# Kernel tuning notes

Hardware: AMD Instinct MI355X
Metric: run time of the kernel (lower is better)

The kernel has to match this reference:

```python
import jax, jax.numpy as jnp
import numpy as np

B, L = 2, 1024
V, D_MODEL, NL = 32, 256, 6
DI, DS, DC, DTR = 512, 16, 4, 16  # d_inner=expand*d_model, d_state, d_conv, dt_rank=d_model/16
NC, MAXL = 10, 2048
ALPHA = 0.1  # observer_alpha


def setup_inputs() -> dict:
    key = jax.random.key(0)
    ks = jax.random.split(key, 16)
    std = 0.02
    emb = std * jax.random.normal(ks[0], (V, D_MODEL), jnp.float32)
    emb = emb.at[0].set(0.0)  # padding_idx=0
    pos_emb = std * jax.random.normal(ks[1], (MAXL, D_MODEL), jnp.float32)
    ln_w = jnp.ones((NL, D_MODEL), jnp.float32)
    ln_b = jnp.zeros((NL, D_MODEL), jnp.float32)
    in_proj_w = std * jax.random.normal(ks[2], (NL, 2 * DI, D_MODEL), jnp.float32)
    conv_w = 0.1 * jax.random.normal(ks[3], (NL, DI, DC), jnp.float32)
    conv_b = jnp.zeros((NL, DI), jnp.float32)
    x_proj_w = std * jax.random.normal(ks[4], (NL, DTR + 2 * DS, DI), jnp.float32)
    dt_proj_w = std * jax.random.normal(ks[5], (NL, DI, DTR), jnp.float32)
    dt_proj_b = jnp.full((NL, DI), -4.6, jnp.float32)  # softplus(-4.6) ~ 0.01 init dt
    A_log = jnp.broadcast_to(jnp.log(jnp.arange(1, DS + 1, dtype=jnp.float32)), (NL, DI, DS)).copy()  # S4D-real
    Dp = jnp.ones((NL, DI), jnp.float32)
    out_proj_w = std * jax.random.normal(ks[6], (NL, D_MODEL, DI), jnp.float32)
    norm_w = jnp.ones((D_MODEL,), jnp.float32)
    norm_b = jnp.zeros((D_MODEL,), jnp.float32)
    cls_w = std * jax.random.normal(ks[7], (NC, D_MODEL), jnp.float32)
    cls_b = jnp.zeros((NC,), jnp.float32)
    x = jax.random.randint(ks[8], (B, L), 0, V, jnp.int64 if jax.config.jax_enable_x64 else jnp.int32)
    mask = jnp.ones((B, L), jnp.int32)
    return dict(emb=emb, pos_emb=pos_emb, ln_w=ln_w, ln_b=ln_b, in_proj_w=in_proj_w,
                conv_w=conv_w, conv_b=conv_b, x_proj_w=x_proj_w, dt_proj_w=dt_proj_w,
                dt_proj_b=dt_proj_b, A_log=A_log, Dp=Dp, out_proj_w=out_proj_w,
                norm_w=norm_w, norm_b=norm_b, cls_w=cls_w, cls_b=cls_b, x=x, mask=mask)


def _ln(x, w, b):
    m = x.mean(-1, keepdims=True)
    v = ((x - m) ** 2).mean(-1, keepdims=True)
    return (x - m) / jnp.sqrt(v + 1e-5) * w + b


def _forward(emb, pos_emb, ln_w, ln_b, in_proj_w, conv_w, conv_b, x_proj_w,
             dt_proj_w, dt_proj_b, A_log, Dp, out_proj_w, norm_w, norm_b,
             cls_w, cls_b, x, mask):
    Bsz, Lsz = x.shape
    h = emb[x] + pos_emb[:Lsz][None, :, :]  # [B,L,D]
    for i in range(NL):
        res = h
        hn = _ln(h, ln_w[i], ln_b[i])
        xz = hn @ in_proj_w[i].T                      # [B,L,2*DI]
        x_in, z = jnp.split(xz, 2, axis=-1)
        # causal depthwise conv1d, kernel DC
        xpad = jnp.pad(x_in, ((0, 0), (DC - 1, 0), (0, 0)))
        xc = conv_b[i]
        for k in range(DC):
            xc = xc + conv_w[i][:, k] * xpad[:, k:k + Lsz, :]
        xc = jax.nn.silu(xc)
        x_dbl = xc @ x_proj_w[i].T                    # [B,L,DTR+2*DS]
        dt = x_dbl[..., :DTR]
        Bm = x_dbl[..., DTR:DTR + DS]
        Cm = x_dbl[..., DTR + DS:]
        delta = jax.nn.softplus(dt @ dt_proj_w[i].T + dt_proj_b[i])  # [B,L,DI]
        A = -jnp.exp(A_log[i])                        # [DI,DS]
        dA = jnp.exp(delta[..., None] * A)            # [B,L,DI,DS]
        dBu = delta[..., None] * Bm[:, :, None, :] * xc[..., None]

        def step(carry, inp):
            hs, hh = carry
            dA_t, dBu_t, c_t = inp
            hs = dA_t * hs + dBu_t                    # true state
            pred = dA_t * hh + dBu_t                  # observer prediction
            hh = pred + ALPHA * (hs - pred)           # Luenberger correction
            y = jnp.einsum('bdn,bn->bd', hh, c_t)
            return (hs, hh), y

        init = (jnp.zeros((Bsz, DI, DS), xc.dtype), jnp.zeros((Bsz, DI, DS), xc.dtype))
        _, ys = jax.lax.scan(step, init,
                             (jnp.moveaxis(dA, 1, 0), jnp.moveaxis(dBu, 1, 0), jnp.moveaxis(Cm, 1, 0)))
        y = jnp.moveaxis(ys, 0, 1) + Dp[i] * xc       # [B,L,DI]
        y = y * jax.nn.silu(z)
        h = y @ out_proj_w[i].T + res
    mf = mask[..., None].astype(h.dtype)
    pooled = (h * mf).sum(axis=1) / mf.sum(axis=1)    # masked mean pool
    pooled = _ln(pooled, norm_w, norm_b)
    return pooled @ cls_w.T + cls_b                   # [B,NC]


def reference(emb, pos_emb, ln_w, ln_b, in_proj_w, conv_w, conv_b, x_proj_w,
              dt_proj_w, dt_proj_b, A_log, Dp, out_proj_w, norm_w, norm_b,
              cls_w, cls_b, x, mask):
    return _forward(emb, pos_emb, ln_w, ln_b, in_proj_w, conv_w, conv_b, x_proj_w,
                    dt_proj_w, dt_proj_b, A_log, Dp, out_proj_w, norm_w, norm_b,
                    cls_w, cls_b, x, mask)
```

## Files before the change

### kernel.cpp

```cpp
#include <hip/hip_runtime.h>
#include <math.h>

#define B_ 2
#define L_ 1024
#define DM 256
#define NL_ 6
#define DI_ 512
#define DS_ 16
#define DC_ 4
#define NC_ 10
#define ALPHA_ 0.1f
#define LC 32
#define NCH (L_/LC)
#define NCHAIN (B_*DI_*DS_)
#define BETA_LC 0.034336838202925124f

typedef unsigned short ushort_t;
typedef __attribute__((ext_vector_type(8))) short s16x8;
typedef __attribute__((ext_vector_type(4))) float f32x4;
typedef __attribute__((ext_vector_type(8))) unsigned short u16x8;

__device__ __forceinline__ float sigmoidf_(float x){ return 1.f/(1.f+__expf(-x)); }
__device__ __forceinline__ ushort_t f2bf(float f){
  union{float f;unsigned u;} c; c.f=f; unsigned u=c.u;
  return (ushort_t)((u + 0x7fffu + ((u>>16)&1u))>>16);
}
__device__ __forceinline__ float bf2f(ushort_t h){
  union{unsigned u;float f;} c; c.u = ((unsigned)h)<<16; return c.f;
}
__device__ __forceinline__ int kidx(int d){ return d + ((d>>7)<<2); }

__global__ void k_embed(const float* __restrict__ emb, const float* __restrict__ pos,
                        const int* __restrict__ ids, float* __restrict__ h){
  int row = blockIdx.x;
  int t = row & (L_-1);
  int d = threadIdx.x;
  int v = ids[row];
  h[(size_t)row*DM + d] = emb[(size_t)v*DM + d] + pos[(size_t)t*DM + d];
}

__global__ void k_cvt2(const float* __restrict__ a, int na, const float* __restrict__ b2,
                       ushort_t* __restrict__ oa, ushort_t* __restrict__ ob, int ntot){
  int i = (blockIdx.x*256 + threadIdx.x)*4;
  if (i >= ntot) return;
  const float* src; ushort_t* dst; int k;
  if (i < na){ src = a; dst = oa; k = i; }
  else       { src = b2; dst = ob; k = i - na; }
  float4 v = *reinterpret_cast<const float4*>(&src[k]);
  ushort4 r;
  r.x = f2bf(v.x); r.y = f2bf(v.y); r.z = f2bf(v.z); r.w = f2bf(v.w);
  *reinterpret_cast<ushort4*>(&dst[k]) = r;
}

__global__ __launch_bounds__(256) void k_gemm_ln(const float* __restrict__ h,
    const ushort_t* __restrict__ W, const float* __restrict__ lw,
    const float* __restrict__ lb, ushort_t* __restrict__ xzb){
  __shared__ ushort_t As[64][264];
  __shared__ ushort_t Ws[64][264];
  int bm = blockIdx.y<<6, bn = blockIdx.x<<6;
  int tid = threadIdx.x;
  {
    int r = tid>>2, q = tid&3;
    const float* src = &h[(size_t)(bm+r)*DM + q*64];
    float4 v[16]; float s1=0.f, s2=0.f;
    #pragma unroll
    for (int i=0;i<16;i++){
      v[i] = *reinterpret_cast<const float4*>(src + i*4);
      s1 += v[i].x+v[i].y+v[i].z+v[i].w;
      s2 += v[i].x*v[i].x+v[i].y*v[i].y+v[i].z*v[i].z+v[i].w*v[i].w;
    }
    s1 += __shfl_xor(s1,1); s2 += __shfl_xor(s2,1);
    s1 += __shfl_xor(s1,2); s2 += __shfl_xor(s2,2);
    float mean = s1*(1.f/DM);
    float rstd = rsqrtf(s2*(1.f/DM) - mean*mean + 1e-5f);
    #pragma unroll
    for (int i=0;i<16;i++){
      int c = q*64 + i*4;
      ushort4 o;
      o.x = f2bf((v[i].x-mean)*rstd*lw[c+0]+lb[c+0]);
      o.y = f2bf((v[i].y-mean)*rstd*lw[c+1]+lb[c+1]);
      o.z = f2bf((v[i].z-mean)*rstd*lw[c+2]+lb[c+2]);
      o.w = f2bf((v[i].w-mean)*rstd*lw[c+3]+lb[c+3]);
      *reinterpret_cast<ushort4*>(&As[r][c]) = o;
    }
    const ushort_t* ws = &W[(size_t)(bn+r)*DM + q*64];
    #pragma unroll
    for (int i=0;i<8;i++)
      *reinterpret_cast<u16x8*>(&Ws[r][q*64+i*8]) = *reinterpret_cast<const u16x8*>(ws + i*8);
  }
  __syncthreads();
  int lane = tid&63, wid = tid>>6;
  int wm = (wid>>1)<<5, wn = (wid&1)<<5;
  int fr = lane&15, fk = (lane>>4)<<3;
  f32x4 acc[2][2] = {};
  #pragma unroll
  for (int k0=0;k0<DM;k0+=32){
    s16x8 a0 = *reinterpret_cast<const s16x8*>(&As[wm+fr][k0+fk]);
    s16x8 a1 = *reinterpret_cast<const s16x8*>(&As[wm+16+fr][k0+fk]);
    s16x8 b0 = *reinterpret_cast<const s16x8*>(&Ws[wn+fr][k0+fk]);
    s16x8 b1 = *reinterpret_cast<const s16x8*>(&Ws[wn+16+fr][k0+fk]);
    acc[0][0] = __builtin_amdgcn_mfma_f32_16x16x32_bf16(a0,b0,acc[0][0],0,0,0);
    acc[0][1] = __builtin_amdgcn_mfma_f32_16x16x32_bf16(a0,b1,acc[0][1],0,0,0);
    acc[1][0] = __builtin_amdgcn_mfma_f32_16x16x32_bf16(a1,b0,acc[1][0],0,0,0);
    acc[1][1] = __builtin_amdgcn_mfma_f32_16x16x32_bf16(a1,b1,acc[1][1],0,0,0);
  }
  int cr = (lane>>4)<<2, cc = lane&15;
  #pragma unroll
  for (int i=0;i<2;i++)
    #pragma unroll
    for (int j=0;j<2;j++){
      int row = bm + wm + (i<<4) + cr;
      int col = bn + wn + (j<<4) + cc;
      #pragma unroll
      for (int r=0;r<4;r++)
        xzb[(size_t)(row+r)*(2*DI_) + col] = f2bf(acc[i][j][r]);
    }
}

__global__ __launch_bounds__(256) void k_xpc(const ushort_t* __restrict__ xzb,
    const float* __restrict__ cw, const float* __restrict__ cb,
    const float* __restrict__ xw, const float* __restrict__ dtw,
    const float* __restrict__ dtb, ushort_t* __restrict__ xcb,
    float* __restrict__ xdbl, ushort_t* __restrict__ deltab){
  __shared__ float sxz[7][DI_];
  __shared__ float sx[4][DI_+16];
  __shared__ float sdbl[4][48];
  int tid = threadIdx.x;
  int m0 = blockIdx.x*4;
  #pragma unroll
  for (int idx=0; idx<14; ++idx){
    int flat = idx*256 + tid;
    int i = flat>>9, d = flat&511;
    int mr = m0 - 3 + i;
    sxz[i][d] = (mr>=0) ? bf2f(xzb[(size_t)mr*(2*DI_) + d]) : 0.f;
  }
  __syncthreads();
  #pragma unroll
  for (int idx=0; idx<8; ++idx){
    int flat = idx*256 + tid;
    int r = flat>>9, d = flat&511;
    int t = (m0 + r) & (L_-1);
    float acc = cb[d];
    #pragma unroll
    for (int k=0;k<4;k++)
      if (t-3+k >= 0) acc = fmaf(cw[d*4+k], sxz[r+k][d], acc);
    float sv = acc * sigmoidf_(acc);
    sx[r][kidx(d)] = sv;
    xcb[(size_t)(m0+r)*DI_ + d] = f2bf(sv);
  }
  __syncthreads();
  if (tid < 192){
    int o = tid>>2, q = tid&3;
    const float* wp = &xw[(size_t)o*DI_ + q*128];
    const int qb = q*132;
    float a0=0.f,a1=0.f,a2=0.f,a3=0.f;
    #pragma unroll 8
    for (int k4=0;k4<32;k4++){
      float4 wv = *reinterpret_cast<const float4*>(wp + k4*4);
      int kk = qb + k4*4;
      float4 x0 = *reinterpret_cast<const float4*>(&sx[0][kk]);
      float4 x1 = *reinterpret_cast<const float4*>(&sx[1][kk]);
      float4 x2 = *reinterpret_cast<const float4*>(&sx[2][kk]);
      float4 x3 = *reinterpret_cast<const float4*>(&sx[3][kk]);
      a0 = fmaf(x0.x,wv.x,a0); a0 = fmaf(x0.y,wv.y,a0); a0 = fmaf(x0.z,wv.z,a0); a0 = fmaf(x0.w,wv.w,a0);
      a1 = fmaf(x1.x,wv.x,a1); a1 = fmaf(x1.y,wv.y,a1); a1 = fmaf(x1.z,wv.z,a1); a1 = fmaf(x1.w,wv.w,a1);
      a2 = fmaf(x2.x,wv.x,a2); a2 = fmaf(x2.y,wv.y,a2); a2 = fmaf(x2.z,wv.z,a2); a2 = fmaf(x2.w,wv.w,a2);
      a3 = fmaf(x3.x,wv.x,a3); a3 = fmaf(x3.y,wv.y,a3); a3 = fmaf(x3.z,wv.z,a3); a3 = fmaf(x3.w,wv.w,a3);
    }
    a0 += __shfl_xor(a0,1); a0 += __shfl_xor(a0,2);
    a1 += __shfl_xor(a1,1); a1 += __shfl_xor(a1,2);
    a2 += __shfl_xor(a2,1); a2 += __shfl_xor(a2,2);
    a3 += __shfl_xor(a3,1); a3 += __shfl_xor(a3,2);
    if (q==0){
      sdbl[0][o]=a0; sdbl[1][o]=a1; sdbl[2][o]=a2; sdbl[3][o]=a3;
      xdbl[(size_t)(m0+0)*48+o]=a0;
      xdbl[(size_t)(m0+1)*48+o]=a1;
      xdbl[(size_t)(m0+2)*48+o]=a2;
      xdbl[(size_t)(m0+3)*48+o]=a3;
    }
  }
  __syncthreads();
  #pragma unroll
  for (int idx=0; idx<8; ++idx){
    int flat = idx*256 + tid;
    int r = flat>>9, n = flat&511;
    const float4* wp = reinterpret_cast<const float4*>(&dtw[n*16]);
    float4 w0=wp[0], w1=wp[1], w2=wp[2], w3=wp[3];
    const float* sd = sdbl[r];
    float acc = dtb[n];
    acc = fmaf(sd[0],w0.x,acc);  acc = fmaf(sd[1],w0.y,acc);
    acc = fmaf(sd[2],w0.z,acc);  acc = fmaf(sd[3],w0.w,acc);
    acc = fmaf(sd[4],w1.x,acc);  acc = fmaf(sd[5],w1.y,acc);
    acc = fmaf(sd[6],w1.z,acc);  acc = fmaf(sd[7],w1.w,acc);
    acc = fmaf(sd[8],w2.x,acc);  acc = fmaf(sd[9],w2.y,acc);
    acc = fmaf(sd[10],w2.z,acc); acc = fmaf(sd[11],w2.w,acc);
    acc = fmaf(sd[12],w3.x,acc); acc = fmaf(sd[13],w3.y,acc);
    acc = fmaf(sd[14],w3.z,acc); acc = fmaf(sd[15],w3.w,acc);
    float sp2 = (acc>20.f)? acc : log1pf(__expf(acc));
    deltab[(size_t)(m0+r)*DI_ + n] = f2bf(sp2);
  }
}

__global__ __launch_bounds__(256) void k_scanA(const ushort_t* __restrict__ deltab,
    const ushort_t* __restrict__ xcb, const float* __restrict__ xdbl,
    const float* __restrict__ A_log, float4* __restrict__ smry){
  int j = blockIdx.x, g = blockIdx.y, b = blockIdx.z;
  int tid = threadIdx.x;
  int n = tid&15, dg = tid>>4;
  int d0 = g*16;
  __shared__ float sdel[LC][16], sxv[LC][16], sB[LC][16];
  if (tid < 128){
    int arr = tid>>6, slot = tid&63, row = slot>>1, half = slot&1;
    int m = b*L_ + j*LC + row;
    const ushort_t* src = arr ? xcb : deltab;
    u16x8 v = *reinterpret_cast<const u16x8*>(&src[(size_t)m*DI_ + d0 + half*8]);
    float* dst = arr ? &sxv[row][half*8] : &sdel[row][half*8];
    #pragma unroll
    for (int i=0;i<8;i++) dst[i] = bf2f((ushort_t)v[i]);
  } else {
    int slot = tid-128;
    int row = slot>>2, c4 = (slot&3)<<2;
    int m = b*L_ + j*LC + row;
    *reinterpret_cast<float4*>(&sB[row][c4]) =
      *reinterpret_cast<const float4*>(&xdbl[(size_t)m*48 + 16 + c4]);
  }
  __syncthreads();
  float a = -__expf(A_log[(d0+dg)*DS_ + n]);
  float hs=0.f, hh=0.f, cp=1.f;
  #pragma unroll
  for (int tt=0; tt<LC; tt+=8){
    float dA8[8], dBu8[8];
    #pragma unroll
    for (int t=0;t<8;t++){
      float dv = sdel[tt+t][dg];
      dA8[t]  = __expf(dv*a);
      dBu8[t] = dv * sxv[tt+t][dg] * sB[tt+t][n];
    }
    #pragma unroll
    for (int t=0;t<8;t++){
      float mix = fmaf(ALPHA_, hs-hh, hh);
      hs = fmaf(dA8[t], hs, dBu8[t]);
      hh = fmaf(dA8[t], mix, dBu8[t]);
      cp *= dA8[t];
    }
  }
  smry[(size_t)j*NCHAIN + (size_t)(b*DI_+d0)*DS_ + tid] = float4{cp,hs,hh,0.f};
}

__global__ __launch_bounds__(256) void k_scanC(const ushort_t* __restrict__ deltab,
    const ushort_t* __restrict__ xcb, const float* __restrict__ xdbl,
    const ushort_t* __restrict__ xzb, const float* __restrict__ A_log,
    const float* __restrict__ Dp, const float4* __restrict__ smry,
    ushort_t* __restrict__ y2b){
  int j = blockIdx.x, g = blockIdx.y, b = blockIdx.z;
  int tid = threadIdx.x;
  int n = tid&15, dg = tid>>4;
  int d0 = g*16;
  __shared__ float sdel[LC][16], sxv[LC][16], sB[LC][16], sC[LC][16], sz[LC][16], sy[LC][16];
  if (tid < 128){
    int arr = tid>>6, slot = tid&63, row = slot>>1, half = slot&1;
    int m = b*L_ + j*LC + row;
    const ushort_t* src = arr ? xcb : deltab;
    u16x8 v = *reinterpret_cast<const u16x8*>(&src[(size_t)m*DI_ + d0 + half*8]);
    float* dst = arr ? &sxv[row][half*8] : &sdel[row][half*8];
    #pragma unroll
    for (int i=0;i<8;i++) dst[i] = bf2f((ushort_t)v[i]);
  } else if (tid < 192){
    int slot = tid-128, row = slot>>1, half = slot&1;
    int m = b*L_ + j*LC + row;
    u16x8 v = *reinterpret_cast<const u16x8*>(&xzb[(size_t)m*(2*DI_) + DI_ + d0 + half*8]);
    #pragma unroll
    for (int i=0;i<8;i++) sz[row][half*8+i] = bf2f((ushort_t)v[i]);
  } else {
    int slot = tid-192;
    #pragma unroll
    for (int k=0;k<4;k++){
      int t4 = slot + k*64;
      int arr = t4>>7, idx4 = t4&127;
      int row = idx4>>2, c4 = (idx4&3)<<2;
      int m = b*L_ + j*LC + row;
      float* dst = arr ? &sC[row][c4] : &sB[row][c4];
      *reinterpret_cast<float4*>(dst) =
        *reinterpret_cast<const float4*>(&xdbl[(size_t)m*48 + 16 + arr*16 + c4]);
    }
  }
  int chain = (b*DI_+d0)*DS_ + tid;
  float hs=0.f, hh=0.f;
  #pragma unroll 4
  for (int jj=0; jj<j; ++jj){
    float4 v = smry[(size_t)jj*NCHAIN + chain];
    float snew = fmaf(v.x, hs, v.y);
    hh = fmaf(v.x, fmaf(BETA_LC, hh-hs, hs), v.z);
    hs = snew;
  }
  __syncthreads();
  float a = -__expf(A_log[(d0+dg)*DS_ + n]);
  #pragma unroll
  for (int tt=0; tt<LC; tt+=8){
    float dA8[8], dBu8[8], yv8[8];
    #pragma unroll
    for (int t=0;t<8;t++){
      float dv = sdel[tt+t][dg];
      dA8[t]  = __expf(dv*a);
      dBu8[t] = dv * sxv[tt+t][dg] * sB[tt+t][n];
    }
    #pragma unroll
    for (int t=0;t<8;t++){
      float mix = fmaf(ALPHA_, hs-hh, hh);
      hs = fmaf(dA8[t], hs, dBu8[t]);
      hh = fmaf(dA8[t], mix, dBu8[t]);
      yv8[t] = hh * sC[tt+t][n];
    }
    #pragma unroll
    for (int t=0;t<8;t++){
      yv8[t] += __shfl_xor(yv8[t],1,16);
      yv8[t] += __shfl_xor(yv8[t],2,16);
      yv8[t] += __shfl_xor(yv8[t],4,16);
      yv8[t] += __shfl_xor(yv8[t],8,16);
    }
    if (n==0){
      #pragma unroll
      for (int t=0;t<8;t++) sy[tt+t][dg] = yv8[t];
    }
  }
  __syncthreads();
  float dpv = Dp[d0 + (tid&15)];
  #pragma unroll
  for (int idx=0; idx<2; ++idx){
    int flat = idx*256 + tid;
    int t2 = flat>>4, dd = flat&15;
    float xvv = sxv[t2][dd];
    float zv  = sz [t2][dd];
    float yfin = (sy[t2][dd] + dpv*xvv) * (zv*sigmoidf_(zv));
    y2b[(size_t)(b*L_ + j*LC + t2)*DI_ + d0 + dd] = f2bf(yfin);
  }
}

__global__ __launch_bounds__(256) void k_gemm_out(const ushort_t* __restrict__ A,
    const ushort_t* __restrict__ W, float* __restrict__ h){
  __shared__ ushort_t As[32][264];
  __shared__ ushort_t Ws[64][264];
  int bm = blockIdx.y<<5, bn = blockIdx.x<<6;
  int tid = threadIdx.x;
  int lane = tid&63, wid = tid>>6;
  int wm = (wid>>1)<<4, wn = (wid&1)<<5;
  int fr = lane&15, fk = (lane>>4)<<3;
  f32x4 acc[2] = {};
  for (int k0=0;k0<DI_;k0+=256){
    {
      int r = tid>>3, q = tid&7;
      const ushort_t* src = &A[(size_t)(bm+r)*DI_ + k0 + q*32];
      #pragma unroll
      for (int i=0;i<4;i++)
        *reinterpret_cast<u16x8*>(&As[r][q*32+i*8]) = *reinterpret_cast<const u16x8*>(src+i*8);
      int r2 = tid>>2, q2 = tid&3;
      const ushort_t* ws = &W[(size_t)(bn+r2)*DI_ + k0 + q2*64];
      #pragma unroll
      for (int i=0;i<8;i++)
        *reinterpret_cast<u16x8*>(&Ws[r2][q2*64+i*8]) = *reinterpret_cast<const u16x8*>(ws+i*8);
    }
    __syncthreads();
    #pragma unroll
    for (int k=0;k<256;k+=32){
      s16x8 a0 = *reinterpret_cast<const s16x8*>(&As[wm+fr][k+fk]);
      s16x8 b0 = *reinterpret_cast<const s16x8*>(&Ws[wn+fr][k+fk]);
      s16x8 b1 = *reinterpret_cast<const s16x8*>(&Ws[wn+16+fr][k+fk]);
      acc[0] = __builtin_amdgcn_mfma_f32_16x16x32_bf16(a0,b0,acc[0],0,0,0);
      acc[1] = __builtin_amdgcn_mfma_f32_16x16x32_bf16(a0,b1,acc[1],0,0,0);
    }
    __syncthreads();
  }
  int cr = (lane>>4)<<2, cc = lane&15;
  #pragma unroll
  for (int jj=0;jj<2;jj++){
    int row = bm + wm + cr;
    int col = bn + wn + (jj<<4) + cc;
    #pragma unroll
    for (int r=0;r<4;r++){
      size_t idx2 = (size_t)(row+r)*DM + col;
      h[idx2] += acc[jj][r];
    }
  }
}

__global__ __launch_bounds__(256) void k_pool(const float* __restrict__ h,
    const int* __restrict__ mask, float* __restrict__ partial){
  int p = blockIdx.x, b = blockIdx.y, d = threadIdx.x;
  int t0 = p*64;
  __shared__ float sm[64];
  if (d < 64) sm[d] = (float)mask[b*L_ + t0 + d];
  __syncthreads();
  const float* hp = &h[(size_t)(b*L_ + t0)*DM + d];
  float s = 0.f;
  #pragma unroll 8
  for (int i=0;i<64;i++)
    s = fmaf(sm[i], hp[(size_t)i*DM], s);
  partial[(size_t)(b*16+p)*DM + d] = s;
}

__global__ __launch_bounds__(256) void k_head(const float* __restrict__ partial,
    const int* __restrict__ mask, const float* __restrict__ nw, const float* __restrict__ nb,
    const float* __restrict__ cw, const float* __restrict__ cb, float* __restrict__ out){
  int b = blockIdx.x, d = threadIdx.x;
  int4 mi = *reinterpret_cast<const int4*>(&mask[b*L_ + d*4]);
  float cnt = (float)(mi.x + mi.y + mi.z + mi.w);
  #pragma unroll
  for (int o=32;o>0;o>>=1) cnt += __shfl_down(cnt,o);
  __shared__ float ac[4];
  __shared__ float scnt;
  int wid = d>>6, lane = d&63;
  if (lane==0) ac[wid] = cnt;
  __syncthreads();
  if (d==0) scnt = ac[0]+ac[1]+ac[2]+ac[3];
  __syncthreads();
  float s = 0.f;
  #pragma unroll
  for (int p=0;p<16;p++) s += partial[(size_t)(b*16+p)*DM + d];
  float v = s / scnt;
  float s1 = v, s2 = v*v;
  #pragma unroll
  for (int o=32;o>0;o>>=1){ s1 += __shfl_down(s1,o); s2 += __shfl_down(s2,o); }
  __shared__ float a1[4], a2[4];
  __shared__ float mv[2];
  if (lane==0){ a1[wid]=s1; a2[wid]=s2; }
  __syncthreads();
  if (d==0){
    float t1=a1[0]+a1[1]+a1[2]+a1[3];
    float t2=a2[0]+a2[1]+a2[2]+a2[3];
    float m = t1/(float)DM;
    mv[0]=m; mv[1]=rsqrtf(t2/(float)DM - m*m + 1e-5f);
  }
  __syncthreads();
  __shared__ float sp[DM];
  sp[d] = (v-mv[0])*mv[1]*nw[d]+nb[d];
  __syncthreads();
  __shared__ float cpart[NC_][16];
  if (d < NC_*16){
    int c = d>>4, q = d&15;
    float acc = 0.f;
    #pragma unroll
    for (int k=0;k<16;k++) acc = fmaf(sp[q*16+k], cw[(size_t)c*DM+q*16+k], acc);
    cpart[c][q] = acc;
  }
  __syncthreads();
  if (d < NC_){
    float acc = cb[d];
    #pragma unroll
    for (int q=0;q<16;q++) acc += cpart[d][q];
    out[b*NC_+d] = acc;
  }
}

extern "C" void kernel_launch(void* const* d_in, const int* in_sizes, int n_in,
                              void* d_out, int out_size, void* d_ws, size_t ws_size,
                              hipStream_t stream){
  const float* emb   = (const float*)d_in[0];
  const float* pos   = (const float*)d_in[1];
  const float* ln_w  = (const float*)d_in[2];
  const float* ln_b  = (const float*)d_in[3];
  const float* ipw   = (const float*)d_in[4];
  const float* cw    = (const float*)d_in[5];
  const float* cb    = (const float*)d_in[6];
  const float* xpw   = (const float*)d_in[7];
  const float* dtw   = (const float*)d_in[8];
  const float* dtb   = (const float*)d_in[9];
  const float* A_log = (const float*)d_in[10];
  const float* Dp    = (const float*)d_in[11];
  const float* opw   = (const float*)d_in[12];
  const float* nw    = (const float*)d_in[13];
  const float* nb    = (const float*)d_in[14];
  const float* clw   = (const float*)d_in[15];
  const float* clb   = (const float*)d_in[16];
  const int*   ids   = (const int*)d_in[17];
  const int*   mask  = (const int*)d_in[18];
  float* out = (float*)d_out;

  float* ws    = (float*)d_ws;
  float* h     = ws;
  float* xdbl  = h + 524288;
  float* part  = xdbl + 98304;
  float4* smry = (float4*)(part + 8192);
  ushort_t* xzb    = (ushort_t*)((float*)smry + 2097152);
  ushort_t* xcb    = xzb + 2097152;
  ushort_t* deltab = xcb + 1048576;
  ushort_t* y2b    = deltab + 1048576;
  ushort_t* ipwb   = y2b + 1048576;
  ushort_t* opwb   = ipwb + 1572864;

  const int NA = 6*2*DI_*DM, NB = 6*DM*DI_;
  k_cvt2<<<dim3((NA+NB)/1024), 256, 0, stream>>>(ipw, NA, opw, ipwb, opwb, NA+NB);
  k_embed<<<dim3(B_*L_), dim3(DM), 0, stream>>>(emb, pos, ids, h);

  for (int l=0; l<NL_; ++l){
    k_gemm_ln<<<dim3(16, 32), 256, 0, stream>>>(
        h, ipwb + (size_t)l*2*DI_*DM, ln_w + l*DM, ln_b + l*DM, xzb);
    k_xpc<<<dim3((B_*L_)/4), 256, 0, stream>>>(
        xzb, cw + l*DI_*DC_, cb + l*DI_, xpw + (size_t)l*48*DI_,
        dtw + (size_t)l*DI_*16, dtb + l*DI_, xcb, xdbl, deltab);
    k_scanA<<<dim3(NCH, DI_/16, B_), 256, 0, stream>>>(
        deltab, xcb, xdbl, A_log + (size_t)l*DI_*DS_, smry);
    k_scanC<<<dim3(NCH, DI_/16, B_), 256, 0, stream>>>(
        deltab, xcb, xdbl, xzb, A_log + (size_t)l*DI_*DS_, Dp + l*DI_,
        smry, y2b);
    k_gemm_out<<<dim3(DM/64, (B_*L_)/32), 256, 0, stream>>>(
        y2b, opwb + (size_t)l*DM*DI_, h);
  }
  k_pool<<<dim3(16, B_), 256, 0, stream>>>(h, mask, part);
  k_head<<<dim3(B_), 256, 0, stream>>>(part, mask, nw, nb, clw, clb, out);
}
```

Before: 477.3 us.

## Fuse dt projection into scan kernels and add separate chunk-prefix scan kernel

Removes the delta (softplus dt_proj) computation and its bf16 buffer from k_xpc, and recomputes delta inside both k_scanA and k_scanC from the shared-memory xdbl tile and dt weights. Adds a k_scanB kernel that does the sequential cross-chunk prefix once per chain and stores the initial states, instead of each k_scanC block replaying up to 31 chunk summaries. Also vectorizes the xzb loads and xcb stores in k_xpc to 8-wide. In exchange, delta is computed twice, there is one extra launch per layer, and an initial-state array is written and read.

```diff
diff --git a/kernel.cpp b/kernel.cpp
--- a/kernel.cpp
+++ b/kernel.cpp
@@ -119,34 +119,45 @@
 
 __global__ __launch_bounds__(256) void k_xpc(const ushort_t* __restrict__ xzb,
     const float* __restrict__ cw, const float* __restrict__ cb,
-    const float* __restrict__ xw, const float* __restrict__ dtw,
-    const float* __restrict__ dtb, ushort_t* __restrict__ xcb,
-    float* __restrict__ xdbl, ushort_t* __restrict__ deltab){
+    const float* __restrict__ xw, ushort_t* __restrict__ xcb,
+    float* __restrict__ xdbl){
   __shared__ float sxz[7][DI_];
   __shared__ float sx[4][DI_+16];
-  __shared__ float sdbl[4][48];
   int tid = threadIdx.x;
   int m0 = blockIdx.x*4;
   #pragma unroll
-  for (int idx=0; idx<14; ++idx){
-    int flat = idx*256 + tid;
-    int i = flat>>9, d = flat&511;
-    int mr = m0 - 3 + i;
-    sxz[i][d] = (mr>=0) ? bf2f(xzb[(size_t)mr*(2*DI_) + d]) : 0.f;
-  }
-  __syncthreads();
-  #pragma unroll
-  for (int idx=0; idx<8; ++idx){
-    int flat = idx*256 + tid;
-    int r = flat>>9, d = flat&511;
+  for (int q=0;q<2;q++){
+    int idx = q*256 + tid;
+    if (idx < 448){
+      int i = idx>>6, c8 = (idx&63)<<3;
+      int mr = m0 - 3 + i;
+      if (mr >= 0){
+        u16x8 v = *reinterpret_cast<const u16x8*>(&xzb[(size_t)mr*(2*DI_) + c8]);
+        #pragma unroll
+        for (int e=0;e<8;e++) sxz[i][c8+e] = bf2f((ushort_t)v[e]);
+      } else {
+        #pragma unroll
+        for (int e=0;e<8;e++) sxz[i][c8+e] = 0.f;
+      }
+    }
+  }
+  __syncthreads();
+  {
+    int r = tid>>6, c8 = (tid&63)<<3;
     int t = (m0 + r) & (L_-1);
-    float acc = cb[d];
-    #pragma unroll
-    for (int k=0;k<4;k++)
-      if (t-3+k >= 0) acc = fmaf(cw[d*4+k], sxz[r+k][d], acc);
-    float sv = acc * sigmoidf_(acc);
-    sx[r][kidx(d)] = sv;
-    xcb[(size_t)(m0+r)*DI_ + d] = f2bf(sv);
+    u16x8 outv;
+    #pragma unroll
+    for (int e=0;e<8;e++){
+      int d = c8 + e;
+      float acc = cb[d];
+      #pragma unroll
+      for (int k=0;k<4;k++)
+        if (t-3+k >= 0) acc = fmaf(cw[d*4+k], sxz[r+k][d], acc);
+      float sv = acc * sigmoidf_(acc);
+      sx[r][kidx(d)] = sv;
+      outv[e] = (short)f2bf(sv);
+    }
+    *reinterpret_cast<u16x8*>(&xcb[(size_t)(m0+r)*DI_ + c8]) = outv;
   }
   __syncthreads();
   if (tid < 192){
@@ -172,57 +183,51 @@
     a2 += __shfl_xor(a2,1); a2 += __shfl_xor(a2,2);
     a3 += __shfl_xor(a3,1); a3 += __shfl_xor(a3,2);
     if (q==0){
-      sdbl[0][o]=a0; sdbl[1][o]=a1; sdbl[2][o]=a2; sdbl[3][o]=a3;
       xdbl[(size_t)(m0+0)*48+o]=a0;
       xdbl[(size_t)(m0+1)*48+o]=a1;
       xdbl[(size_t)(m0+2)*48+o]=a2;
       xdbl[(size_t)(m0+3)*48+o]=a3;
     }
   }
-  __syncthreads();
-  #pragma unroll
-  for (int idx=0; idx<8; ++idx){
-    int flat = idx*256 + tid;
-    int r = flat>>9, n = flat&511;
-    const float4* wp = reinterpret_cast<const float4*>(&dtw[n*16]);
-    float4 w0=wp[0], w1=wp[1], w2=wp[2], w3=wp[3];
-    const float* sd = sdbl[r];
-    float acc = dtb[n];
-    acc = fmaf(sd[0],w0.x,acc);  acc = fmaf(sd[1],w0.y,acc);
-    acc = fmaf(sd[2],w0.z,acc);  acc = fmaf(sd[3],w0.w,acc);
-    acc = fmaf(sd[4],w1.x,acc);  acc = fmaf(sd[5],w1.y,acc);
-    acc = fmaf(sd[6],w1.z,acc);  acc = fmaf(sd[7],w1.w,acc);
-    acc = fmaf(sd[8],w2.x,acc);  acc = fmaf(sd[9],w2.y,acc);
-    acc = fmaf(sd[10],w2.z,acc); acc = fmaf(sd[11],w2.w,acc);
-    acc = fmaf(sd[12],w3.x,acc); acc = fmaf(sd[13],w3.y,acc);
-    acc = fmaf(sd[14],w3.z,acc); acc = fmaf(sd[15],w3.w,acc);
-    float sp2 = (acc>20.f)? acc : log1pf(__expf(acc));
-    deltab[(size_t)(m0+r)*DI_ + n] = f2bf(sp2);
-  }
-}
-
-__global__ __launch_bounds__(256) void k_scanA(const ushort_t* __restrict__ deltab,
-    const ushort_t* __restrict__ xcb, const float* __restrict__ xdbl,
-    const float* __restrict__ A_log, float4* __restrict__ smry){
+}
+
+__global__ __launch_bounds__(256) void k_scanA(const ushort_t* __restrict__ xcb,
+    const float* __restrict__ xdbl, const float* __restrict__ dtw,
+    const float* __restrict__ dtb, const float* __restrict__ A_log,
+    float4* __restrict__ smry){
   int j = blockIdx.x, g = blockIdx.y, b = blockIdx.z;
   int tid = threadIdx.x;
   int n = tid&15, dg = tid>>4;
   int d0 = g*16;
-  __shared__ float sdel[LC][16], sxv[LC][16], sB[LC][16];
-  if (tid < 128){
-    int arr = tid>>6, slot = tid&63, row = slot>>1, half = slot&1;
-    int m = b*L_ + j*LC + row;
-    const ushort_t* src = arr ? xcb : deltab;
-    u16x8 v = *reinterpret_cast<const u16x8*>(&src[(size_t)m*DI_ + d0 + half*8]);
-    float* dst = arr ? &sxv[row][half*8] : &sdel[row][half*8];
-    #pragma unroll
-    for (int i=0;i<8;i++) dst[i] = bf2f((ushort_t)v[i]);
-  } else {
-    int slot = tid-128;
-    int row = slot>>2, c4 = (slot&3)<<2;
-    int m = b*L_ + j*LC + row;
-    *reinterpret_cast<float4*>(&sB[row][c4]) =
-      *reinterpret_cast<const float4*>(&xdbl[(size_t)m*48 + 16 + c4]);
+  int mbase = b*L_ + j*LC;
+  __shared__ float sbd[LC][48];
+  __shared__ float sdtw[16][16];
+  __shared__ float sxv[LC][16];
+  __shared__ float sdel[LC][16];
+  {
+    const float4* xsrc = reinterpret_cast<const float4*>(xdbl + (size_t)mbase*48);
+    reinterpret_cast<float4*>(&sbd[0][0])[tid] = xsrc[tid];
+    if (tid < 128) reinterpret_cast<float4*>(&sbd[0][0])[256+tid] = xsrc[256+tid];
+    if (tid < 64){
+      int row = tid>>1, half = tid&1;
+      u16x8 v = *reinterpret_cast<const u16x8*>(&xcb[(size_t)(mbase+row)*DI_ + d0 + half*8]);
+      #pragma unroll
+      for (int e=0;e<8;e++) sxv[row][half*8+e] = bf2f((ushort_t)v[e]);
+    } else if (tid < 128){
+      int s = tid-64, row = s>>2, c4 = (s&3)<<2;
+      *reinterpret_cast<float4*>(&sdtw[row][c4]) =
+        *reinterpret_cast<const float4*>(&dtw[(size_t)(d0+row)*16 + c4]);
+    }
+  }
+  __syncthreads();
+  #pragma unroll
+  for (int q=0;q<2;q++){
+    int p = q*256 + tid;
+    int t = p>>4, dd = p&15;
+    float acc = dtb[d0+dd];
+    #pragma unroll
+    for (int k=0;k<16;k++) acc = fmaf(sbd[t][k], sdtw[dd][k], acc);
+    sdel[t][dd] = (acc>20.f)? acc : log1pf(__expf(acc));
   }
   __syncthreads();
   float a = -__expf(A_log[(d0+dg)*DS_ + n]);
@@ -234,7 +239,7 @@
     for (int t=0;t<8;t++){
       float dv = sdel[tt+t][dg];
       dA8[t]  = __expf(dv*a);
-      dBu8[t] = dv * sxv[tt+t][dg] * sB[tt+t][n];
+      dBu8[t] = dv * sxv[tt+t][dg] * sbd[tt+t][16+n];
     }
     #pragma unroll
     for (int t=0;t<8;t++){
@@ -247,54 +252,73 @@
   smry[(size_t)j*NCHAIN + (size_t)(b*DI_+d0)*DS_ + tid] = float4{cp,hs,hh,0.f};
 }
 
-__global__ __launch_bounds__(256) void k_scanC(const ushort_t* __restrict__ deltab,
-    const ushort_t* __restrict__ xcb, const float* __restrict__ xdbl,
-    const ushort_t* __restrict__ xzb, const float* __restrict__ A_log,
-    const float* __restrict__ Dp, const float4* __restrict__ smry,
-    ushort_t* __restrict__ y2b){
+__global__ __launch_bounds__(256) void k_scanB(const float4* __restrict__ smry,
+    float2* __restrict__ initArr){
+  int g = blockIdx.x, b = blockIdx.y;
+  int c = (b*DI_ + g*16)*DS_ + threadIdx.x;
+  float hs=0.f, hh=0.f;
+  #pragma unroll
+  for (int j=0;j<NCH;j++){
+    size_t o = (size_t)j*NCHAIN + c;
+    float4 v = smry[o];
+    initArr[o] = float2{hs,hh};
+    float snew = fmaf(v.x, hs, v.y);
+    hh = fmaf(v.x, fmaf(BETA_LC, hh-hs, hs), v.z);
+    hs = snew;
+  }
+}
+
+__global__ __launch_bounds__(256) void k_scanC(const ushort_t* __restrict__ xcb,
+    const float* __restrict__ xdbl, const ushort_t* __restrict__ xzb,
+    const float* __restrict__ dtw, const float* __restrict__ dtb,
+    const float* __restrict__ A_log, const float* __restrict__ Dp,
+    const float2* __restrict__ initArr, ushort_t* __restrict__ y2b){
   int j = blockIdx.x, g = blockIdx.y, b = blockIdx.z;
   int tid = threadIdx.x;
   int n = tid&15, dg = tid>>4;
   int d0 = g*16;
-  __shared__ float sdel[LC][16], sxv[LC][16], sB[LC][16], sC[LC][16], sz[LC][16], sy[LC][16];
-  if (tid < 128){
-    int arr = tid>>6, slot = tid&63, row = slot>>1, half = slot&1;
-    int m = b*L_ + j*LC + row;
-    const ushort_t* src = arr ? xcb : deltab;
-    u16x8 v = *reinterpret_cast<const u16x8*>(&src[(size_t)m*DI_ + d0 + half*8]);
-    float* dst = arr ? &sxv[row][half*8] : &sdel[row][half*8];
-    #pragma unroll
-    for (int i=0;i<8;i++) dst[i] = bf2f((ushort_t)v[i]);
-  } else if (tid < 192){
-    int slot = tid-128, row = slot>>1, half = slot&1;
-    int m = b*L_ + j*LC + row;
-    u16x8 v = *reinterpret_cast<const u16x8*>(&xzb[(size_t)m*(2*DI_) + DI_ + d0 + half*8]);
-    #pragma unroll
-    for (int i=0;i<8;i++) sz[row][half*8+i] = bf2f((ushort_t)v[i]);
-  } else {
-    int slot = tid-192;
-    #pragma unroll
-    for (int k=0;k<4;k++){
-      int t4 = slot + k*64;
-      int arr = t4>>7, idx4 = t4&127;
-      int row = idx4>>2, c4 = (idx4&3)<<2;
-      int m = b*L_ + j*LC + row;
-      float* dst = arr ? &sC[row][c4] : &sB[row][c4];
-      *reinterpret_cast<float4*>(dst) =
-        *reinterpret_cast<const float4*>(&xdbl[(size_t)m*48 + 16 + arr*16 + c4]);
-    }
-  }
+  int mbase = b*L_ + j*LC;
   int chain = (b*DI_+d0)*DS_ + tid;
-  float hs=0.f, hh=0.f;
-  #pragma unroll 4
-  for (int jj=0; jj<j; ++jj){
-    float4 v = smry[(size_t)jj*NCHAIN + chain];
-    float snew = fmaf(v.x, hs, v.y);
-    hh = fmaf(v.x, fmaf(BETA_LC, hh-hs, hs), v.z);
-    hs = snew;
+  float2 iv = initArr[(size_t)j*NCHAIN + chain];
+  __shared__ float sbd[LC][48];
+  __shared__ float sdtw[16][16];
+  __shared__ float sxv[LC][16];
+  __shared__ float sdel[LC][16];
+  __shared__ float sz[LC][16];
+  __shared__ float sy[LC][16];
+  {
+    const float4* xsrc = reinterpret_cast<const float4*>(xdbl + (size_t)mbase*48);
+    reinterpret_cast<float4*>(&sbd[0][0])[tid] = xsrc[tid];
+    if (tid < 128) reinterpret_cast<float4*>(&sbd[0][0])[256+tid] = xsrc[256+tid];
+    if (tid < 64){
+      int row = tid>>1, half = tid&1;
+      u16x8 v = *reinterpret_cast<const u16x8*>(&xcb[(size_t)(mbase+row)*DI_ + d0 + half*8]);
+      #pragma unroll
+      for (int e=0;e<8;e++) sxv[row][half*8+e] = bf2f((ushort_t)v[e]);
+    } else if (tid < 128){
+      int s = tid-64, row = s>>1, half = s&1;
+      u16x8 v = *reinterpret_cast<const u16x8*>(&xzb[(size_t)(mbase+row)*(2*DI_) + DI_ + d0 + half*8]);
+      #pragma unroll
+      for (int e=0;e<8;e++) sz[row][half*8+e] = bf2f((ushort_t)v[e]);
+    } else if (tid < 192){
+      int s = tid-128, row = s>>2, c4 = (s&3)<<2;
+      *reinterpret_cast<float4*>(&sdtw[row][c4]) =
+        *reinterpret_cast<const float4*>(&dtw[(size_t)(d0+row)*16 + c4]);
+    }
+  }
+  __syncthreads();
+  #pragma unroll
+  for (int q=0;q<2;q++){
+    int p = q*256 + tid;
+    int t = p>>4, dd = p&15;
+    float acc = dtb[d0+dd];
+    #pragma unroll
+    for (int k=0;k<16;k++) acc = fmaf(sbd[t][k], sdtw[dd][k], acc);
+    sdel[t][dd] = (acc>20.f)? acc : log1pf(__expf(acc));
   }
   __syncthreads();
   float a = -__expf(A_log[(d0+dg)*DS_ + n]);
+  float hs = iv.x, hh = iv.y;
   #pragma unroll
   for (int tt=0; tt<LC; tt+=8){
     float dA8[8], dBu8[8], yv8[8];
@@ -302,14 +326,14 @@
     for (int t=0;t<8;t++){
       float dv = sdel[tt+t][dg];
       dA8[t]  = __expf(dv*a);
-      dBu8[t] = dv * sxv[tt+t][dg] * sB[tt+t][n];
+      dBu8[t] = dv * sxv[tt+t][dg] * sbd[tt+t][16+n];
     }
     #pragma unroll
     for (int t=0;t<8;t++){
       float mix = fmaf(ALPHA_, hs-hh, hh);
       hs = fmaf(dA8[t], hs, dBu8[t]);
       hh = fmaf(dA8[t], mix, dBu8[t]);
-      yv8[t] = hh * sC[tt+t][n];
+      yv8[t] = hh * sbd[tt+t][32+n];
     }
     #pragma unroll
     for (int t=0;t<8;t++){
@@ -332,7 +356,7 @@
     float xvv = sxv[t2][dd];
     float zv  = sz [t2][dd];
     float yfin = (sy[t2][dd] + dpv*xvv) * (zv*sigmoidf_(zv));
-    y2b[(size_t)(b*L_ + j*LC + t2)*DI_ + d0 + dd] = f2bf(yfin);
+    y2b[(size_t)(mbase + t2)*DI_ + d0 + dd] = f2bf(yfin);
   }
 }
 
@@ -480,12 +504,12 @@
   float* xdbl  = h + 524288;
   float* part  = xdbl + 98304;
   float4* smry = (float4*)(part + 8192);
-  ushort_t* xzb    = (ushort_t*)((float*)smry + 2097152);
-  ushort_t* xcb    = xzb + 2097152;
-  ushort_t* deltab = xcb + 1048576;
-  ushort_t* y2b    = deltab + 1048576;
-  ushort_t* ipwb   = y2b + 1048576;
-  ushort_t* opwb   = ipwb + 1572864;
+  float2* initA= (float2*)((float*)smry + 2097152);
+  ushort_t* xzb  = (ushort_t*)((float*)initA + 1048576);
+  ushort_t* xcb  = xzb + 2097152;
+  ushort_t* y2b  = xcb + 1048576;
+  ushort_t* ipwb = y2b + 1048576;
+  ushort_t* opwb = ipwb + 1572864;
 
   const int NA = 6*2*DI_*DM, NB = 6*DM*DI_;
   k_cvt2<<<dim3((NA+NB)/1024), 256, 0, stream>>>(ipw, NA, opw, ipwb, opwb, NA+NB);
@@ -495,13 +519,14 @@
     k_gemm_ln<<<dim3(16, 32), 256, 0, stream>>>(
         h, ipwb + (size_t)l*2*DI_*DM, ln_w + l*DM, ln_b + l*DM, xzb);
     k_xpc<<<dim3((B_*L_)/4), 256, 0, stream>>>(
-        xzb, cw + l*DI_*DC_, cb + l*DI_, xpw + (size_t)l*48*DI_,
-        dtw + (size_t)l*DI_*16, dtb + l*DI_, xcb, xdbl, deltab);
+        xzb, cw + l*DI_*DC_, cb + l*DI_, xpw + (size_t)l*48*DI_, xcb, xdbl);
     k_scanA<<<dim3(NCH, DI_/16, B_), 256, 0, stream>>>(
-        deltab, xcb, xdbl, A_log + (size_t)l*DI_*DS_, smry);
+        xcb, xdbl, dtw + (size_t)l*DI_*16, dtb + l*DI_,
+        A_log + (size_t)l*DI_*DS_, smry);
+    k_scanB<<<dim3(DI_/16, B_), 256, 0, stream>>>(smry, initA);
     k_scanC<<<dim3(NCH, DI_/16, B_), 256, 0, stream>>>(
-        deltab, xcb, xdbl, xzb, A_log + (size_t)l*DI_*DS_, Dp + l*DI_,
-        smry, y2b);
+        xcb, xdbl, xzb, dtw + (size_t)l*DI_*16, dtb + l*DI_,
+        A_log + (size_t)l*DI_*DS_, Dp + l*DI_, initA, y2b);
     k_gemm_out<<<dim3(DM/64, (B_*L_)/32), 256, 0, stream>>>(
         y2b, opwb + (size_t)l*DM*DI_, h);
   }
```

Result: no change. 484.6 us (+1.5%).
